# Kernel optimization log

Measured on AMD Instinct MI355X. Metric: run time of the kernel, lower is better.

Reference implementation:

```python
import jax, jax.numpy as jnp
import numpy as np

B, N, M, H, D, DIM = 4, 2048, 512, 12, 64, 768
INNER = H * D
SCALE = D ** -0.5
NEG = -1e9
TEMP = 24.0


def setup_inputs() -> dict:
    key = jax.random.key(0)
    ks = jax.random.split(key, 8)
    x = jax.random.normal(ks[0], (B, N, DIM), jnp.float32)
    kx = jax.random.normal(ks[1], (B, M, DIM), jnp.float32)
    krd = jax.random.uniform(ks[2], (B, H, M, N), jnp.float32)
    clst = jax.random.normal(ks[3], (B, 1, DIM), jnp.float32)
    att_mask = jax.random.randint(ks[4], (B, H, N, M), 0, 2) > 0
    W_qkv = jax.random.normal(ks[5], (DIM, 3 * INNER), jnp.float32) / np.sqrt(DIM)
    W_out = jax.random.normal(ks[6], (INNER, DIM), jnp.float32) / np.sqrt(INNER)
    b_out = jnp.zeros((DIM,), jnp.float32)
    return {"x": x, "kx": kx, "krd": krd, "clst": clst, "att_mask": att_mask,
            "W_qkv": W_qkv, "W_out": W_out, "b_out": b_out}


def _qkv(t, W_qkv):
    # [b, n, dim] -> three [b, h, n, d]
    b, n, _ = t.shape
    qkv = (t @ W_qkv).reshape(b, n, 3, H, D)
    qkv = jnp.moveaxis(qkv, 2, 0)            # [3, b, n, h, d]
    qkv = jnp.transpose(qkv, (0, 1, 3, 2, 4))  # [3, b, h, n, d]
    return qkv[0], qkv[1], qkv[2]


def _merge(t):
    # [b, h, n, d] -> [b, n, h*d]
    b, h, n, d = t.shape
    return jnp.transpose(t, (0, 2, 1, 3)).reshape(b, n, h * d)


def reference(x, kx, krd, clst, att_mask, W_qkv, W_out, b_out):
    t_q, t_k, t_v = _qkv(x, W_qkv)
    k_q, k_k, k_v = _qkv(kx, W_qkv)
    c_q, _, _ = _qkv(clst, W_qkv)

    krd_T = jnp.transpose(krd, (0, 1, 3, 2))  # [b, h, N, M]

    # branch 1: instance queries vs kernel keys
    dots = jnp.einsum('bhid,bhjd->bhij', t_q, k_k) * SCALE
    dots = jnp.where(att_mask, NEG, dots)
    attn_hot = jax.nn.softmax(dots * TEMP, axis=-1) * krd_T
    attn = jax.nn.softmax(dots, axis=-1) * krd_T
    att_out = _merge(jnp.einsum('bhij,bhjd->bhid', attn, k_v))

    # branch 2: kernel queries vs instance keys
    k_dots = jnp.einsum('bhid,bhjd->bhij', k_q, t_k) * SCALE
    k_dots = jnp.where(jnp.transpose(att_mask, (0, 1, 3, 2)), NEG, k_dots)
    k_attn = jax.nn.softmax(k_dots, axis=-1) * krd
    k_out = _merge(jnp.einsum('bhij,bhjd->bhid', k_attn, t_v))

    # branch 3: cluster query vs kernel keys
    c_dots = jnp.einsum('bhid,bhjd->bhij', c_q, k_k) * SCALE
    c_dots = jnp.where(att_mask[:, :, :1], NEG, c_dots)
    c_attn = jax.nn.softmax(c_dots, axis=-1)
    c_out = _merge(jnp.einsum('bhij,bhjd->bhid', c_attn, k_v))

    proj = lambda t: t @ W_out + b_out
    return (proj(att_out), proj(k_out), proj(c_out),
            jnp.transpose(attn_hot, (0, 1, 3, 2)))
```

## Files before the change

kernel.cpp:

```cpp
#include <hip/hip_runtime.h>
#include <hip/hip_bf16.h>
#include <cmath>
#include <cstdint>

#define B_ 4
#define N_ 2048
#define M_ 512
#define H_ 12
#define D_ 64
#define DIM_ 768
#define QKV_ 2304
#define SCALE_ 0.125f
#define NEG_ -1e9f
#define TEMP_ 24.0f
#define NSPLIT_ 4

typedef __attribute__((ext_vector_type(8))) short bf16x8;
typedef __attribute__((ext_vector_type(4))) float f32x4;

__device__ __forceinline__ short f2bf(float f) {
  union { float f; unsigned u; } v; v.f = f;
  unsigned r = v.u + 0x7fffu + ((v.u >> 16) & 1u);
  return (short)(r >> 16);
}
__device__ __forceinline__ float bf2f(short s) {
  union { unsigned u; float f; } v; v.u = ((unsigned)(unsigned short)s) << 16;
  return v.f;
}
#define MFMA16(a, b, c) __builtin_amdgcn_mfma_f32_16x16x32_bf16(a, b, c, 0, 0, 0)

__device__ __forceinline__ int xcd_swizzle(int orig, int nwg) {
  int qd = nwg >> 3, r = nwg & 7;
  int xcd = orig & 7, pos = orig >> 3;
  return (xcd < r ? xcd * (qd + 1) : r * (qd + 1) + (xcd - r) * qd) + pos;
}

__global__ __launch_bounds__(256) void wsplit_t(
    const float* __restrict__ W, int K, int Ncols,
    short* __restrict__ Wt_h, short* __restrict__ Wt_l) {
  __shared__ float t[32][33];
  const int n0 = blockIdx.x * 32, k0 = blockIdx.y * 32;
  const int tid = threadIdx.x;
  for (int e = tid; e < 1024; e += 256) {
    int r = e >> 5, c = e & 31;
    t[r][c] = W[(size_t)(k0 + r) * Ncols + n0 + c];
  }
  __syncthreads();
  for (int e = tid; e < 1024; e += 256) {
    int r = e >> 5, c = e & 31;
    float f = t[c][r];
    short hi = f2bf(f);
    short lo = f2bf(f - bf2f(hi));
    size_t o = (size_t)(n0 + r) * K + k0 + c;
    Wt_h[o] = hi; Wt_l[o] = lo;
  }
}

__global__ __launch_bounds__(256) void fsplit(
    const float* __restrict__ in, short* __restrict__ ho,
    short* __restrict__ lo_, int n4) {
  int stride = gridDim.x * 256;
  for (int i = blockIdx.x * 256 + threadIdx.x; i < n4; i += stride) {
    float4 f = ((const float4*)in)[i];
    short h0 = f2bf(f.x), h1 = f2bf(f.y), h2 = f2bf(f.z), h3 = f2bf(f.w);
    short l0 = f2bf(f.x - bf2f(h0)), l1 = f2bf(f.y - bf2f(h1));
    short l2 = f2bf(f.z - bf2f(h2)), l3 = f2bf(f.w - bf2f(h3));
    ((short4*)ho)[i] = make_short4(h0, h1, h2, h3);
    ((short4*)lo_)[i] = make_short4(l0, l1, l2, l3);
  }
}

__global__ __launch_bounds__(256) void mask_pack(
    const int* __restrict__ mask, unsigned* __restrict__ pm) {
  const size_t total = (size_t)B_ * H_ * N_ * M_;
  const size_t stride = (size_t)gridDim.x * blockDim.x;
  const int lane = threadIdx.x & 63;
  for (size_t i = (size_t)blockIdx.x * blockDim.x + threadIdx.x; i < total;
       i += stride) {
    unsigned long long bal = __ballot(mask[i] != 0);
    if (lane == 0) *(unsigned long long*)(pm + (i >> 5)) = bal;
  }
}

__global__ __launch_bounds__(256) void qkv_mfma(
    const short* __restrict__ Ahp, const short* __restrict__ Alp,
    const short* __restrict__ Wth, const short* __restrict__ Wtl,
    int rowsPerB, int totalRows,
    short* __restrict__ qh, short* __restrict__ ql,
    short* __restrict__ kh, short* __restrict__ kl,
    short* __restrict__ vt) {
  __shared__ __align__(16) short As_h[128 * 40], As_l[128 * 40];
  __shared__ __align__(16) short Bs_h[128 * 40], Bs_l[128 * 40];
  const int nwg = gridDim.x * gridDim.y;
  const int nb = xcd_swizzle(blockIdx.y * gridDim.x + blockIdx.x, nwg);
  const int gx = gridDim.x;
  const int r0 = (nb / gx) * 128, c0 = (nb % gx) * 128;
  const int tid = threadIdx.x;
  const int w = tid >> 6, ln = tid & 63, q = ln >> 4, l15 = ln & 15;
  const int wM = (w & 1) * 64, wN = (w >> 1) * 64;
  const f32x4 z = {0.f, 0.f, 0.f, 0.f};
  f32x4 acc[4][4];
  for (int i = 0; i < 4; i++)
    for (int j = 0; j < 4; j++) acc[i][j] = z;
  for (int k0 = 0; k0 < DIM_; k0 += 32) {
    for (int e = tid; e < 512; e += 256) {
      int row = e >> 2, c = e & 3;
      int ar = r0 + row; if (ar >= totalRows) ar = totalRows - 1;
      size_t ga = (size_t)ar * DIM_ + k0 + c * 8;
      size_t gb = (size_t)(c0 + row) * DIM_ + k0 + c * 8;
      int o = row * 40 + c * 8;
      *(uint4*)(As_h + o) = *(const uint4*)(Ahp + ga);
      *(uint4*)(As_l + o) = *(const uint4*)(Alp + ga);
      *(uint4*)(Bs_h + o) = *(const uint4*)(Wth + gb);
      *(uint4*)(Bs_l + o) = *(const uint4*)(Wtl + gb);
    }
    __syncthreads();
    bf16x8 ah[4], al[4], bhf[4], blf[4];
    for (int mt = 0; mt < 4; mt++) {
      int o = (wM + mt * 16 + l15) * 40 + q * 8;
      ah[mt] = *(const bf16x8*)(As_h + o);
      al[mt] = *(const bf16x8*)(As_l + o);
    }
    for (int nt = 0; nt < 4; nt++) {
      int o = (wN + nt * 16 + l15) * 40 + q * 8;
      bhf[nt] = *(const bf16x8*)(Bs_h + o);
      blf[nt] = *(const bf16x8*)(Bs_l + o);
    }
    for (int mt = 0; mt < 4; mt++)
      for (int nt = 0; nt < 4; nt++) {
        f32x4 c = acc[mt][nt];
        c = MFMA16(ah[mt], bhf[nt], c);
        c = MFMA16(ah[mt], blf[nt], c);
        c = MFMA16(al[mt], bhf[nt], c);
        acc[mt][nt] = c;
      }
    __syncthreads();
  }
  for (int mt = 0; mt < 4; mt++)
    for (int nt = 0; nt < 4; nt++)
      for (int r = 0; r < 4; r++) {
        int gr = r0 + wM + mt * 16 + q * 4 + r;
        if (gr >= totalRows) continue;
        int gc = c0 + wN + nt * 16 + l15;
        int which = gc / DIM_;
        int rem = gc - which * DIM_;
        int hh = rem >> 6, d = rem & 63;
        int b = gr / rowsPerB, n = gr - b * rowsPerB;
        float v = acc[mt][nt][r];
        short hi = f2bf(v);
        if (which == 2) {
          vt[(((size_t)b * H_ + hh) * 64 + d) * rowsPerB + n] = hi;
        } else {
          short lo = f2bf(v - bf2f(hi));
          size_t o = (((size_t)b * H_ + hh) * rowsPerB + n) * 64 + d;
          if (which == 0) { qh[o] = hi; ql[o] = lo; }
          else           { kh[o] = hi; kl[o] = lo; }
        }
      }
}

__global__ __launch_bounds__(256) void proj_mfma(
    const short* __restrict__ Ahp, const short* __restrict__ Alp,
    const short* __restrict__ Bth, const short* __restrict__ Btl,
    const float* __restrict__ bias, float* __restrict__ C, int totalRows) {
  __shared__ __align__(16) short As_h[128 * 40], As_l[128 * 40];
  __shared__ __align__(16) short Bs_h[128 * 40], Bs_l[128 * 40];
  const int nwg = gridDim.x * gridDim.y;
  const int nb = xcd_swizzle(blockIdx.y * gridDim.x + blockIdx.x, nwg);
  const int gx = gridDim.x;
  const int r0 = (nb / gx) * 128, c0 = (nb % gx) * 128;
  const int tid = threadIdx.x;
  const int w = tid >> 6, ln = tid & 63, q = ln >> 4, l15 = ln & 15;
  const int wM = (w & 1) * 64, wN = (w >> 1) * 64;
  const f32x4 z = {0.f, 0.f, 0.f, 0.f};
  f32x4 acc[4][4];
  for (int i = 0; i < 4; i++)
    for (int j = 0; j < 4; j++) acc[i][j] = z;
  for (int k0 = 0; k0 < DIM_; k0 += 32) {
    for (int e = tid; e < 512; e += 256) {
      int row = e >> 2, c = e & 3;
      int ar = r0 + row; if (ar >= totalRows) ar = totalRows - 1;
      size_t ga = (size_t)ar * DIM_ + k0 + c * 8;
      size_t gb = (size_t)(c0 + row) * DIM_ + k0 + c * 8;
      int o = row * 40 + c * 8;
      *(uint4*)(As_h + o) = *(const uint4*)(Ahp + ga);
      *(uint4*)(As_l + o) = *(const uint4*)(Alp + ga);
      *(uint4*)(Bs_h + o) = *(const uint4*)(Bth + gb);
      *(uint4*)(Bs_l + o) = *(const uint4*)(Btl + gb);
    }
    __syncthreads();
    bf16x8 ah[4], al[4], bhf[4], blf[4];
    for (int mt = 0; mt < 4; mt++) {
      int o = (wM + mt * 16 + l15) * 40 + q * 8;
      ah[mt] = *(const bf16x8*)(As_h + o);
      al[mt] = *(const bf16x8*)(As_l + o);
    }
    for (int nt = 0; nt < 4; nt++) {
      int o = (wN + nt * 16 + l15) * 40 + q * 8;
      bhf[nt] = *(const bf16x8*)(Bs_h + o);
      blf[nt] = *(const bf16x8*)(Bs_l + o);
    }
    for (int mt = 0; mt < 4; mt++)
      for (int nt = 0; nt < 4; nt++) {
        f32x4 c = acc[mt][nt];
        c = MFMA16(ah[mt], bhf[nt], c);
        c = MFMA16(ah[mt], blf[nt], c);
        c = MFMA16(al[mt], bhf[nt], c);
        acc[mt][nt] = c;
      }
    __syncthreads();
  }
  for (int mt = 0; mt < 4; mt++)
    for (int nt = 0; nt < 4; nt++)
      for (int r = 0; r < 4; r++) {
        int gr = r0 + wM + mt * 16 + q * 4 + r;
        if (gr >= totalRows) continue;
        int gc = c0 + wN + nt * 16 + l15;
        C[(size_t)gr * DIM_ + gc] = acc[mt][nt][r] + bias[gc];
      }
}

__global__ __launch_bounds__(512, 4) void branch1_mfma(
    const short* __restrict__ tqh, const short* __restrict__ tql,
    const short* __restrict__ kkh, const short* __restrict__ kkl,
    const short* __restrict__ kvt, const float* __restrict__ krd,
    const unsigned* __restrict__ pm, float* __restrict__ out3,
    short* __restrict__ amh, short* __restrict__ aml) {
  __shared__ __align__(16) float sc[32 * 520];
  __shared__ unsigned mskw[512];
  __shared__ float rowM[32], inv1[32], inv2[32];
  short* P2h = (short*)sc;
  short* P2l = P2h + 32 * 520;
  const int b = blockIdx.z, h = blockIdx.y, n0 = blockIdx.x * 32;
  const size_t bhi = (size_t)b * H_ + h;
  const int tid = threadIdx.x;
  const int w = tid >> 6, ln = tid & 63, q = ln >> 4, l15 = ln & 15;
  const float* krd0 = krd + bhi * M_ * N_;
  mskw[tid] = pm[(bhi * N_ + n0) * 16 + tid];
  {
    bf16x8 ah[2][2], al[2][2];
    for (int mt = 0; mt < 2; mt++) {
      const short* ap = tqh + ((bhi * N_ + n0 + mt * 16 + l15) * D_ + q * 8);
      const short* ap2 = tql + ((bhi * N_ + n0 + mt * 16 + l15) * D_ + q * 8);
      ah[mt][0] = *(const bf16x8*)(ap);
      ah[mt][1] = *(const bf16x8*)(ap + 32);
      al[mt][0] = *(const bf16x8*)(ap2);
      al[mt][1] = *(const bf16x8*)(ap2 + 32);
    }
    for (int t = 0; t < 4; t++) {
      int ct = w * 4 + t;
      const short* bp = kkh + ((bhi * M_ + ct * 16 + l15) * D_ + q * 8);
      const short* bp2 = kkl + ((bhi * M_ + ct * 16 + l15) * D_ + q * 8);
      bf16x8 bh0 = *(const bf16x8*)(bp);
      bf16x8 bh1 = *(const bf16x8*)(bp + 32);
      bf16x8 bl0 = *(const bf16x8*)(bp2);
      bf16x8 bl1 = *(const bf16x8*)(bp2 + 32);
      for (int mt = 0; mt < 2; mt++) {
        f32x4 a = {0.f, 0.f, 0.f, 0.f};
        a = MFMA16(ah[mt][0], bh0, a); a = MFMA16(ah[mt][1], bh1, a);
        a = MFMA16(ah[mt][0], bl0, a); a = MFMA16(ah[mt][1], bl1, a);
        a = MFMA16(al[mt][0], bh0, a); a = MFMA16(al[mt][1], bh1, a);
        for (int r = 0; r < 4; r++) {
          int row = mt * 16 + q * 4 + r;
          sc[row * 520 + ((ct * 16 + l15) ^ ((row >> 2) & 7))] = a[r];
        }
      }
    }
  }
  const int pi = tid & 31, pg = tid >> 5;
  float kr[32];
#pragma unroll
  for (int t = 0; t < 32; t++)
    kr[t] = __builtin_nontemporal_load(
        krd0 + (size_t)(pg * 32 + t) * N_ + n0 + pi);
  __syncthreads();
  {
    int i = tid >> 4, jl = tid & 15;
    int sw = (i >> 2) & 7;
    float* scr = sc + i * 520;
    const unsigned* mrow = mskw + i * 16;
    float mx = -INFINITY;
    for (int j = jl; j < M_; j += 16) {
      float dv = scr[j ^ sw];
      dv = ((mrow[j >> 5] >> (j & 31)) & 1) ? NEG_ : dv * SCALE_;
      scr[j ^ sw] = dv;
      mx = fmaxf(mx, dv);
    }
    for (int o = 8; o >= 1; o >>= 1) mx = fmaxf(mx, __shfl_xor(mx, o, 16));
    float s1 = 0.f, s2 = 0.f;
    for (int j = jl; j < M_; j += 16) {
      float e2 = __expf(scr[j ^ sw] - mx);
      scr[j ^ sw] = e2;
      float x2 = e2 * e2, x4 = x2 * x2, x8 = x4 * x4, x16 = x8 * x8;
      s1 += x16 * x8;
      s2 += e2;
    }
    for (int o = 8; o >= 1; o >>= 1) {
      s1 += __shfl_xor(s1, o, 16);
      s2 += __shfl_xor(s2, o, 16);
    }
    if (jl == 0) { inv1[i] = 1.f / s1; inv2[i] = 1.f / s2; }
  }
  __syncthreads();
  {
    float rv[32];
    int sw2 = (pi >> 2) & 7;
#pragma unroll
    for (int t = 0; t < 32; t++)
      rv[t] = sc[pi * 520 + ((pg * 32 + t) ^ sw2)];
    __syncthreads();
    float v1 = inv1[pi], v2 = inv2[pi];
    float* o3 = out3 + bhi * M_ * N_ + n0 + pi;
#pragma unroll
    for (int t = 0; t < 32; t += 2) {
      int j = pg * 32 + t;
      float e2a = rv[t], e2b = rv[t + 1];
      float a2 = e2a * e2a, a4 = a2 * a2, a8 = a4 * a4, a16 = a8 * a8;
      float b2 = e2b * e2b, b4 = b2 * b2, b8 = b4 * b4, b16 = b8 * b8;
      __builtin_nontemporal_store(a16 * a8 * v1 * kr[t], o3 + (size_t)j * N_);
      __builtin_nontemporal_store(b16 * b8 * v1 * kr[t + 1],
                                  o3 + (size_t)(j + 1) * N_);
      float p0 = e2a * v2 * kr[t];
      float p1 = e2b * v2 * kr[t + 1];
      short h0 = f2bf(p0), h1 = f2bf(p1);
      short lo0 = f2bf(p0 - bf2f(h0)), lo1 = f2bf(p1 - bf2f(h1));
      *(short2*)(P2h + pi * 520 + j) = make_short2(h0, h1);
      *(short2*)(P2l + pi * 520 + j) = make_short2(lo0, lo1);
    }
  }
  __syncthreads();
  {
    const int dc = w & 3, nh = w >> 2;
    f32x4 o0 = {0.f, 0.f, 0.f, 0.f}, o1 = {0.f, 0.f, 0.f, 0.f};
    const short* vbase = kvt + ((bhi * 64 + dc * 16 + l15) * (size_t)M_ + q * 8);
    const short* ph = P2h + (nh * 16 + l15) * 520 + q * 8;
    const short* pl = P2l + (nh * 16 + l15) * 520 + q * 8;
    for (int kc = 0; kc < 16; kc += 2) {
      bf16x8 pa0 = *(const bf16x8*)(ph + kc * 32);
      bf16x8 pl0 = *(const bf16x8*)(pl + kc * 32);
      bf16x8 bv0 = *(const bf16x8*)(vbase + kc * 32);
      o0 = MFMA16(pa0, bv0, o0);
      o0 = MFMA16(pl0, bv0, o0);
      bf16x8 pa1 = *(const bf16x8*)(ph + (kc + 1) * 32);
      bf16x8 pl1 = *(const bf16x8*)(pl + (kc + 1) * 32);
      bf16x8 bv1 = *(const bf16x8*)(vbase + (kc + 1) * 32);
      o1 = MFMA16(pa1, bv1, o1);
      o1 = MFMA16(pl1, bv1, o1);
    }
    o0 += o1;
    for (int r = 0; r < 4; r++) {
      float v = o0[r];
      short hi = f2bf(v), lo = f2bf(v - bf2f(hi));
      size_t o = ((size_t)b * N_ + n0 + nh * 16 + q * 4 + r) * DIM_ +
                 h * 64 + dc * 16 + l15;
      amh[o] = hi; aml[o] = lo;
    }
  }
}

__global__ __launch_bounds__(256) void branch2_mfma(
    const short* __restrict__ kqh, const short* __restrict__ kql,
    const short* __restrict__ tkh, const short* __restrict__ tkl,
    const short* __restrict__ tvt, const float* __restrict__ krd,
    const unsigned* __restrict__ pm, float* __restrict__ pO,
    float* __restrict__ pML) {
  __shared__ __align__(16) float sc[32 * 136];
  __shared__ unsigned mskw[128];
  __shared__ float rowM[32], rowL[32], alph[32];
  short* P2h = (short*)sc;
  short* P2l = P2h + 32 * 136;
  const int b = blockIdx.z, h = blockIdx.y;
  const int mblk = blockIdx.x >> 2, split = blockIdx.x & 3;
  const int m0 = mblk * 32;
  const size_t bhi = (size_t)b * H_ + h;
  const int pidx = ((int)bhi * 16 + mblk) * NSPLIT_ + split;
  const int tid = threadIdx.x;
  const int w = tid >> 6, ln = tid & 63, q = ln >> 4, l15 = ln & 15;
  const float* krd0 = krd + (bhi * M_ + m0) * N_;
  const int mword = m0 >> 5;
  bf16x8 Ah[2][2], Al[2][2];
  for (int mt = 0; mt < 2; mt++)
    for (int kc = 0; kc < 2; kc++) {
      size_t o = (bhi * M_ + m0 + mt * 16 + l15) * D_ + kc * 32 + q * 8;
      Ah[mt][kc] = *(const bf16x8*)(kqh + o);
      Al[mt][kc] = *(const bf16x8*)(kql + o);
    }
  if (tid < 32) { rowM[tid] = -INFINITY; rowL[tid] = 0.f; }
  const f32x4 z = {0.f, 0.f, 0.f, 0.f};
  f32x4 oa[2]; oa[0] = z; oa[1] = z;
  __syncthreads();
  const int nbeg = split * (N_ / NSPLIT_), nend = nbeg + N_ / NSPLIT_;
  for (int n0 = nbeg; n0 < nend; n0 += 128) {
    if (tid < 128) mskw[tid] = pm[(bhi * N_ + n0 + tid) * 16 + mword];
    for (int t = 0; t < 2; t++) {
      int ct = w * 2 + t;
      const short* bp = tkh + ((bhi * N_ + n0 + ct * 16 + l15) * D_ + q * 8);
      const short* bp2 = tkl + ((bhi * N_ + n0 + ct * 16 + l15) * D_ + q * 8);
      bf16x8 bh0 = *(const bf16x8*)(bp), bh1 = *(const bf16x8*)(bp + 32);
      bf16x8 bl0 = *(const bf16x8*)(bp2), bl1 = *(const bf16x8*)(bp2 + 32);
      for (int mt = 0; mt < 2; mt++) {
        f32x4 a = {0.f, 0.f, 0.f, 0.f};
        a = MFMA16(Ah[mt][0], bh0, a); a = MFMA16(Ah[mt][1], bh1, a);
        a = MFMA16(Ah[mt][0], bl0, a); a = MFMA16(Ah[mt][1], bl1, a);
        a = MFMA16(Al[mt][0], bh0, a); a = MFMA16(Al[mt][1], bh1, a);
        for (int r = 0; r < 4; r++)
          sc[(mt * 16 + q * 4 + r) * 136 + ct * 16 + l15] = a[r];
      }
    }
    __syncthreads();
    {
      int i = tid >> 3, jl = tid & 7;
      float mx = -INFINITY;
      for (int j = jl; j < 128; j += 8) {
        float s = sc[i * 136 + j];
        s = ((mskw[j] >> i) & 1) ? NEG_ : s * SCALE_;
        sc[i * 136 + j] = s;
        mx = fmaxf(mx, s);
      }
      for (int o = 4; o >= 1; o >>= 1) mx = fmaxf(mx, __shfl_xor(mx, o, 8));
      float mold = rowM[i];
      float mnew = fmaxf(mold, mx);
      float sum = 0.f;
      for (int j = jl; j < 128; j += 8) {
        float p = __expf(sc[i * 136 + j] - mnew);
        sc[i * 136 + j] = p;
        sum += p;
      }
      for (int o = 4; o >= 1; o >>= 1) sum += __shfl_xor(sum, o, 8);
      if (jl == 0) {
        float al = (mold == -INFINITY) ? 0.f : __expf(mold - mnew);
        alph[i] = al;
        rowL[i] = rowL[i] * al + sum;
        rowM[i] = mnew;
      }
    }
    __syncthreads();
    {
      float rv[16], kv2[16];
      const int j = tid & 127;
      const int ib = tid >> 7;
#pragma unroll
      for (int t = 0; t < 16; t++) {
        rv[t] = sc[(ib + 2 * t) * 136 + j];
        kv2[t] = __builtin_nontemporal_load(
            krd0 + (size_t)(ib + 2 * t) * N_ + n0 + j);
      }
      __syncthreads();
#pragma unroll
      for (int t = 0; t < 16; t++) {
        int i = ib + 2 * t;
        float p2 = rv[t] * kv2[t];
        short hi = f2bf(p2), lo = f2bf(p2 - bf2f(hi));
        P2h[i * 136 + j] = hi;
        P2l[i * 136 + j] = lo;
      }
    }
    __syncthreads();
    {
      for (int mt = 0; mt < 2; mt++) {
        f32x4 t = oa[mt];
        for (int r = 0; r < 4; r++) t[r] *= alph[mt * 16 + q * 4 + r];
        for (int kc = 0; kc < 4; kc++) {
          bf16x8 pa = *(const bf16x8*)(P2h + (mt * 16 + l15) * 136 + kc * 32 + q * 8);
          bf16x8 pl = *(const bf16x8*)(P2l + (mt * 16 + l15) * 136 + kc * 32 + q * 8);
          bf16x8 bv = *(const bf16x8*)(tvt + ((bhi * 64 + w * 16 + l15) * (size_t)N_ + n0 + kc * 32 + q * 8));
          t = MFMA16(pa, bv, t);
          t = MFMA16(pl, bv, t);
        }
        oa[mt] = t;
      }
    }
    __syncthreads();
  }
  float* po = pO + (size_t)pidx * 2048;
  for (int mt = 0; mt < 2; mt++)
    for (int r = 0; r < 4; r++) {
      int row = mt * 16 + q * 4 + r;
      po[row * 64 + w * 16 + l15] = oa[mt][r];
    }
  if (tid < 32) {
    pML[(size_t)pidx * 64 + tid] = rowM[tid];
    pML[(size_t)pidx * 64 + 32 + tid] = rowL[tid];
  }
}

__global__ __launch_bounds__(256) void b2_combine(
    const float* __restrict__ pO, const float* __restrict__ pML,
    short* __restrict__ kmh, short* __restrict__ kml) {
  const int mblk = blockIdx.x, h = blockIdx.y, b = blockIdx.z;
  const size_t bhi = (size_t)b * H_ + h;
  const int base = ((int)bhi * 16 + mblk) * NSPLIT_;
  __shared__ float mS[NSPLIT_][32], lS[NSPLIT_][32], wgt[NSPLIT_][32], invL[32];
  const int tid = threadIdx.x;
  if (tid < 32 * NSPLIT_) {
    int s = tid >> 5, r = tid & 31;
    mS[s][r] = pML[(size_t)(base + s) * 64 + r];
    lS[s][r] = pML[(size_t)(base + s) * 64 + 32 + r];
  }
  __syncthreads();
  if (tid < 32) {
    float Mv = mS[0][tid];
    for (int s = 1; s < NSPLIT_; s++) Mv = fmaxf(Mv, mS[s][tid]);
    float L = 0.f;
    for (int s = 0; s < NSPLIT_; s++) {
      float wv = __expf(mS[s][tid] - Mv);
      wgt[s][tid] = wv;
      L += lS[s][tid] * wv;
    }
    invL[tid] = 1.f / L;
  }
  __syncthreads();
  const int row = tid >> 3, c0 = (tid & 7) * 8;
  float acc[8] = {0, 0, 0, 0, 0, 0, 0, 0};
  for (int s = 0; s < NSPLIT_; s++) {
    float wv = wgt[s][row];
    const float* src = pO + (size_t)(base + s) * 2048 + row * 64 + c0;
    float4 a = *(const float4*)(src);
    float4 bq = *(const float4*)(src + 4);
    acc[0] += a.x * wv;  acc[1] += a.y * wv;
    acc[2] += a.z * wv;  acc[3] += a.w * wv;
    acc[4] += bq.x * wv; acc[5] += bq.y * wv;
    acc[6] += bq.z * wv; acc[7] += bq.w * wv;
  }
  float il = invL[row];
  size_t o = ((size_t)b * M_ + mblk * 32 + row) * DIM_ + h * 64 + c0;
#pragma unroll
  for (int e = 0; e < 8; e++) {
    float v = acc[e] * il;
    short hi = f2bf(v), lo = f2bf(v - bf2f(hi));
    kmh[o + e] = hi; kml[o + e] = lo;
  }
}

__global__ __launch_bounds__(256) void branch3_k(
    const short* __restrict__ cqh, const short* __restrict__ cql,
    const short* __restrict__ kkh, const short* __restrict__ kkl,
    const short* __restrict__ kvt, const unsigned* __restrict__ pm,
    short* __restrict__ cmh, short* __restrict__ cml) {
  const int h = blockIdx.x, b = blockIdx.y;
  __shared__ float qv[64];
  __shared__ float p[512];
  __shared__ float wr1[4], wr2[4];
  __shared__ float ored[4][64];
  const size_t bhi = (size_t)b * H_ + h;
  const int tid = threadIdx.x;
  if (tid < 64) qv[tid] = bf2f(cqh[bhi * 64 + tid]) + bf2f(cql[bhi * 64 + tid]);
  __syncthreads();
  const unsigned* m0p = pm + bhi * N_ * 16;
  for (int j = tid; j < 512; j += 256) {
    float acc = 0;
    for (int kk = 0; kk < 64; kk++)
      acc += qv[kk] * (bf2f(kkh[(bhi * M_ + j) * 64 + kk]) +
                       bf2f(kkl[(bhi * M_ + j) * 64 + kk]));
    acc *= SCALE_;
    if ((m0p[j >> 5] >> (j & 31)) & 1) acc = NEG_;
    p[j] = acc;
  }
  __syncthreads();
  float mx = fmaxf(p[tid], p[tid + 256]);
  for (int o = 32; o >= 1; o >>= 1) mx = fmaxf(mx, __shfl_xor(mx, o, 64));
  if ((tid & 63) == 0) wr1[tid >> 6] = mx;
  __syncthreads();
  mx = fmaxf(fmaxf(wr1[0], wr1[1]), fmaxf(wr1[2], wr1[3]));
  float e0 = __expf(p[tid] - mx), e1 = __expf(p[tid + 256] - mx);
  float s = e0 + e1;
  for (int o = 32; o >= 1; o >>= 1) s += __shfl_xor(s, o, 64);
  p[tid] = e0; p[tid + 256] = e1;
  if ((tid & 63) == 0) wr2[tid >> 6] = s;
  __syncthreads();
  float invS = 1.f / (wr2[0] + wr2[1] + wr2[2] + wr2[3]);
  int dd = tid & 63, gg = tid >> 6;
  float o = 0;
  for (int j = gg; j < 512; j += 4)
    o += p[j] * bf2f(kvt[(bhi * 64 + dd) * (size_t)M_ + j]);
  ored[gg][dd] = o;
  __syncthreads();
  if (gg == 0) {
    float r = (ored[0][dd] + ored[1][dd] + ored[2][dd] + ored[3][dd]) * invS;
    short hi = f2bf(r), lo = f2bf(r - bf2f(hi));
    cmh[(size_t)b * DIM_ + h * 64 + dd] = hi;
    cml[(size_t)b * DIM_ + h * 64 + dd] = lo;
  }
}

extern "C" void kernel_launch(void* const* d_in, const int* in_sizes, int n_in,
                              void* d_out, int out_size, void* d_ws,
                              size_t ws_size, hipStream_t stream) {
  const float* x = (const float*)d_in[0];
  const float* kx = (const float*)d_in[1];
  const float* krd = (const float*)d_in[2];
  const float* clst = (const float*)d_in[3];
  const int* mask = (const int*)d_in[4];
  const float* Wqkv = (const float*)d_in[5];
  const float* Wout = (const float*)d_in[6];
  const float* bout = (const float*)d_in[7];

  short* p = (short*)d_ws;
  auto alloc = [&](size_t n) { short* r = p; p += n; return r; };
  short* Wq_h = alloc(2304ull * 768); short* Wq_l = alloc(2304ull * 768);
  short* Wo_h = alloc(768ull * 768);  short* Wo_l = alloc(768ull * 768);
  short* tq_h = alloc(6291456); short* tq_l = alloc(6291456);
  short* tk_h = alloc(6291456); short* tk_l = alloc(6291456);
  short* tv_t = alloc(6291456);
  short* kq_h = alloc(1572864); short* kq_l = alloc(1572864);
  short* kk_h = alloc(1572864); short* kk_l = alloc(1572864);
  short* kv_t = alloc(1572864);
  short* cq_h = alloc(3072); short* cq_l = alloc(3072);
  short* ck_h = alloc(3072); short* ck_l = alloc(3072);
  short* cv_t = alloc(3072);
  short* am_h = alloc(6291456); short* am_l = alloc(6291456);
  short* km_h = alloc(1572864); short* km_l = alloc(1572864);
  short* cm_h = alloc(3072); short* cm_l = alloc(3072);

  float* out0 = (float*)d_out;
  float* out1 = out0 + 6291456;
  float* out2 = out1 + 1572864;
  float* out3 = out2 + 3072;

  wsplit_t<<<dim3(72, 24), 256, 0, stream>>>(Wqkv, DIM_, QKV_, Wq_h, Wq_l);
  wsplit_t<<<dim3(24, 24), 256, 0, stream>>>(Wout, DIM_, DIM_, Wo_h, Wo_l);

  short* xs_h = am_h, *xs_l = am_l;
  short* kxs_h = km_h, *kxs_l = km_l;
  short* cs_h = cm_h, *cs_l = cm_l;
  fsplit<<<dim3(2048), 256, 0, stream>>>(x, xs_h, xs_l, B_ * N_ * DIM_ / 4);
  fsplit<<<dim3(1536), 256, 0, stream>>>(kx, kxs_h, kxs_l, B_ * M_ * DIM_ / 4);
  fsplit<<<dim3(3), 256, 0, stream>>>(clst, cs_h, cs_l, B_ * DIM_ / 4);

  qkv_mfma<<<dim3(18, 64), 256, 0, stream>>>(xs_h, xs_l, Wq_h, Wq_l, N_,
                                             B_ * N_, tq_h, tq_l, tk_h, tk_l,
                                             tv_t);
  qkv_mfma<<<dim3(18, 16), 256, 0, stream>>>(kxs_h, kxs_l, Wq_h, Wq_l, M_,
                                             B_ * M_, kq_h, kq_l, kk_h, kk_l,
                                             kv_t);
  qkv_mfma<<<dim3(18, 1), 256, 0, stream>>>(cs_h, cs_l, Wq_h, Wq_l, 1, B_,
                                            cq_h, cq_l, ck_h, ck_l, cv_t);

  unsigned* pmask = (unsigned*)Wq_h;
  mask_pack<<<dim3(2048), 256, 0, stream>>>(mask, pmask);

  branch1_mfma<<<dim3(N_ / 32, H_, B_), 512, 0, stream>>>(
      tq_h, tq_l, kk_h, kk_l, kv_t, krd, pmask, out3, am_h, am_l);

  float* pO = out0;
  float* pML = out1;
  branch2_mfma<<<dim3((M_ / 32) * NSPLIT_, H_, B_), 256, 0, stream>>>(
      kq_h, kq_l, tk_h, tk_l, tv_t, krd, pmask, pO, pML);
  b2_combine<<<dim3(M_ / 32, H_, B_), 256, 0, stream>>>(pO, pML, km_h, km_l);

  branch3_k<<<dim3(H_, B_), 256, 0, stream>>>(cq_h, cq_l, kk_h, kk_l, kv_t,
                                              pmask, cm_h, cm_l);

  proj_mfma<<<dim3(6, 64), 256, 0, stream>>>(am_h, am_l, Wo_h, Wo_l, bout,
                                             out0, B_ * N_);
  proj_mfma<<<dim3(6, 16), 256, 0, stream>>>(km_h, km_l, Wo_h, Wo_l, bout,
                                             out1, B_ * M_);
  proj_mfma<<<dim3(6, 1), 256, 0, stream>>>(cm_h, cm_l, Wo_h, Wo_l, bout,
                                            out2, B_);
}
```

Before: 1.168 ms.

## Merge launches, use direct global-to-LDS loads, double branch-2 splits

```diff
diff --git a/kernel.cpp b/kernel.cpp
--- a/kernel.cpp
+++ b/kernel.cpp
@@ -13,7 +13,7 @@
 #define SCALE_ 0.125f
 #define NEG_ -1e9f
 #define TEMP_ 24.0f
-#define NSPLIT_ 4
+#define NSPLIT_ 8
 
 typedef __attribute__((ext_vector_type(8))) short bf16x8;
 typedef __attribute__((ext_vector_type(4))) float f32x4;
@@ -29,17 +29,29 @@
 }
 #define MFMA16(a, b, c) __builtin_amdgcn_mfma_f32_16x16x32_bf16(a, b, c, 0, 0, 0)
 
+__device__ __forceinline__ void gl16(const void* g, void* l) {
+  __builtin_amdgcn_global_load_lds(
+      (const __attribute__((address_space(1))) unsigned int*)g,
+      (__attribute__((address_space(3))) unsigned int*)l, 16, 0, 0);
+}
+
 __device__ __forceinline__ int xcd_swizzle(int orig, int nwg) {
   int qd = nwg >> 3, r = nwg & 7;
   int xcd = orig & 7, pos = orig >> 3;
   return (xcd < r ? xcd * (qd + 1) : r * (qd + 1) + (xcd - r) * qd) + pos;
 }
 
-__global__ __launch_bounds__(256) void wsplit_t(
-    const float* __restrict__ W, int K, int Ncols,
-    short* __restrict__ Wt_h, short* __restrict__ Wt_l) {
+__global__ __launch_bounds__(256) void wsplit_all(
+    const float* __restrict__ Wqkv, const float* __restrict__ Wout,
+    short* __restrict__ Wqh, short* __restrict__ Wql,
+    short* __restrict__ Woh, short* __restrict__ Wol) {
   __shared__ float t[32][33];
-  const int n0 = blockIdx.x * 32, k0 = blockIdx.y * 32;
+  int bx = blockIdx.x;
+  const float* W; int Ncols; short *Wh, *Wl;
+  if (bx < 72) { W = Wqkv; Ncols = QKV_; Wh = Wqh; Wl = Wql; }
+  else { bx -= 72; W = Wout; Ncols = DIM_; Wh = Woh; Wl = Wol; }
+  const int K = DIM_;
+  const int n0 = bx * 32, k0 = blockIdx.y * 32;
   const int tid = threadIdx.x;
   for (int e = tid; e < 1024; e += 256) {
     int r = e >> 5, c = e & 31;
@@ -52,21 +64,32 @@
     short hi = f2bf(f);
     short lo = f2bf(f - bf2f(hi));
     size_t o = (size_t)(n0 + r) * K + k0 + c;
-    Wt_h[o] = hi; Wt_l[o] = lo;
-  }
-}
-
-__global__ __launch_bounds__(256) void fsplit(
-    const float* __restrict__ in, short* __restrict__ ho,
-    short* __restrict__ lo_, int n4) {
+    Wh[o] = hi; Wl[o] = lo;
+  }
+}
+
+__global__ __launch_bounds__(256) void fsplit_all(
+    const float* __restrict__ x, const float* __restrict__ kx,
+    const float* __restrict__ c,
+    short* __restrict__ xh, short* __restrict__ xl,
+    short* __restrict__ kh2, short* __restrict__ kl2,
+    short* __restrict__ ch, short* __restrict__ cl) {
+  const int XN4 = B_ * N_ * DIM_ / 4;
+  const int KN4 = B_ * M_ * DIM_ / 4;
+  const int CN4 = B_ * DIM_ / 4;
+  const int total = XN4 + KN4 + CN4;
   int stride = gridDim.x * 256;
-  for (int i = blockIdx.x * 256 + threadIdx.x; i < n4; i += stride) {
-    float4 f = ((const float4*)in)[i];
+  for (int i = blockIdx.x * 256 + threadIdx.x; i < total; i += stride) {
+    const float* src; short *ho, *lo2; int idx;
+    if (i < XN4) { src = x; ho = xh; lo2 = xl; idx = i; }
+    else if (i < XN4 + KN4) { src = kx; ho = kh2; lo2 = kl2; idx = i - XN4; }
+    else { src = c; ho = ch; lo2 = cl; idx = i - XN4 - KN4; }
+    float4 f = ((const float4*)src)[idx];
     short h0 = f2bf(f.x), h1 = f2bf(f.y), h2 = f2bf(f.z), h3 = f2bf(f.w);
     short l0 = f2bf(f.x - bf2f(h0)), l1 = f2bf(f.y - bf2f(h1));
     short l2 = f2bf(f.z - bf2f(h2)), l3 = f2bf(f.w - bf2f(h3));
-    ((short4*)ho)[i] = make_short4(h0, h1, h2, h3);
-    ((short4*)lo_)[i] = make_short4(l0, l1, l2, l3);
+    ((short4*)ho)[idx] = make_short4(h0, h1, h2, h3);
+    ((short4*)lo2)[idx] = make_short4(l0, l1, l2, l3);
   }
 }
 
@@ -82,19 +105,36 @@
   }
 }
 
-__global__ __launch_bounds__(256) void qkv_mfma(
-    const short* __restrict__ Ahp, const short* __restrict__ Alp,
+__global__ __launch_bounds__(256) void qkv_all(
+    const short* __restrict__ xsh, const short* __restrict__ xsl,
+    const short* __restrict__ kxsh, const short* __restrict__ kxsl,
+    const short* __restrict__ csh, const short* __restrict__ csl,
     const short* __restrict__ Wth, const short* __restrict__ Wtl,
-    int rowsPerB, int totalRows,
-    short* __restrict__ qh, short* __restrict__ ql,
-    short* __restrict__ kh, short* __restrict__ kl,
-    short* __restrict__ vt) {
-  __shared__ __align__(16) short As_h[128 * 40], As_l[128 * 40];
-  __shared__ __align__(16) short Bs_h[128 * 40], Bs_l[128 * 40];
-  const int nwg = gridDim.x * gridDim.y;
-  const int nb = xcd_swizzle(blockIdx.y * gridDim.x + blockIdx.x, nwg);
-  const int gx = gridDim.x;
-  const int r0 = (nb / gx) * 128, c0 = (nb % gx) * 128;
+    short* __restrict__ tqh, short* __restrict__ tql,
+    short* __restrict__ tkh, short* __restrict__ tkl, short* __restrict__ tvt,
+    short* __restrict__ kqh, short* __restrict__ kql,
+    short* __restrict__ kkh, short* __restrict__ kkl, short* __restrict__ kvt,
+    short* __restrict__ cqh, short* __restrict__ cql,
+    short* __restrict__ ckh, short* __restrict__ ckl, short* __restrict__ cvt) {
+  __shared__ __align__(16) short As_h[128 * 32], As_l[128 * 32];
+  __shared__ __align__(16) short Bs_h[128 * 32], Bs_l[128 * 32];
+  int flat = blockIdx.y * 18 + blockIdx.x;
+  flat = xcd_swizzle(flat, 18 * 81);
+  int by = flat / 18, bx = flat % 18;
+  const short *Ahp, *Alp; int rowsPerB, totalRows, r0;
+  short *qh, *ql, *kh, *kl, *vt;
+  if (by < 64) {
+    Ahp = xsh; Alp = xsl; rowsPerB = N_; totalRows = B_ * N_; r0 = by * 128;
+    qh = tqh; ql = tql; kh = tkh; kl = tkl; vt = tvt;
+  } else if (by < 80) {
+    Ahp = kxsh; Alp = kxsl; rowsPerB = M_; totalRows = B_ * M_;
+    r0 = (by - 64) * 128;
+    qh = kqh; ql = kql; kh = kkh; kl = kkl; vt = kvt;
+  } else {
+    Ahp = csh; Alp = csl; rowsPerB = 1; totalRows = B_; r0 = 0;
+    qh = cqh; ql = cql; kh = ckh; kl = ckl; vt = cvt;
+  }
+  const int c0 = bx * 128;
   const int tid = threadIdx.x;
   const int w = tid >> 6, ln = tid & 63, q = ln >> 4, l15 = ln & 15;
   const int wM = (w & 1) * 64, wN = (w >> 1) * 64;
@@ -108,31 +148,30 @@
       int ar = r0 + row; if (ar >= totalRows) ar = totalRows - 1;
       size_t ga = (size_t)ar * DIM_ + k0 + c * 8;
       size_t gb = (size_t)(c0 + row) * DIM_ + k0 + c * 8;
-      int o = row * 40 + c * 8;
-      *(uint4*)(As_h + o) = *(const uint4*)(Ahp + ga);
-      *(uint4*)(As_l + o) = *(const uint4*)(Alp + ga);
-      *(uint4*)(Bs_h + o) = *(const uint4*)(Wth + gb);
-      *(uint4*)(Bs_l + o) = *(const uint4*)(Wtl + gb);
+      gl16(Ahp + ga, As_h + e * 8);
+      gl16(Alp + ga, As_l + e * 8);
+      gl16(Wth + gb, Bs_h + e * 8);
+      gl16(Wtl + gb, Bs_l + e * 8);
     }
     __syncthreads();
     bf16x8 ah[4], al[4], bhf[4], blf[4];
     for (int mt = 0; mt < 4; mt++) {
-      int o = (wM + mt * 16 + l15) * 40 + q * 8;
+      int o = (wM + mt * 16 + l15) * 32 + q * 8;
       ah[mt] = *(const bf16x8*)(As_h + o);
       al[mt] = *(const bf16x8*)(As_l + o);
     }
     for (int nt = 0; nt < 4; nt++) {
-      int o = (wN + nt * 16 + l15) * 40 + q * 8;
+      int o = (wN + nt * 16 + l15) * 32 + q * 8;
       bhf[nt] = *(const bf16x8*)(Bs_h + o);
       blf[nt] = *(const bf16x8*)(Bs_l + o);
     }
     for (int mt = 0; mt < 4; mt++)
       for (int nt = 0; nt < 4; nt++) {
-        f32x4 c = acc[mt][nt];
-        c = MFMA16(ah[mt], bhf[nt], c);
-        c = MFMA16(ah[mt], blf[nt], c);
-        c = MFMA16(al[mt], bhf[nt], c);
-        acc[mt][nt] = c;
+        f32x4 cc = acc[mt][nt];
+        cc = MFMA16(ah[mt], bhf[nt], cc);
+        cc = MFMA16(ah[mt], blf[nt], cc);
+        cc = MFMA16(al[mt], bhf[nt], cc);
+        acc[mt][nt] = cc;
       }
     __syncthreads();
   }
@@ -159,16 +198,23 @@
       }
 }
 
-__global__ __launch_bounds__(256) void proj_mfma(
-    const short* __restrict__ Ahp, const short* __restrict__ Alp,
+__global__ __launch_bounds__(256) void proj_all(
+    const short* __restrict__ amh, const short* __restrict__ aml,
+    const short* __restrict__ kmh, const short* __restrict__ kml,
+    const short* __restrict__ cmh, const short* __restrict__ cml,
     const short* __restrict__ Bth, const short* __restrict__ Btl,
-    const float* __restrict__ bias, float* __restrict__ C, int totalRows) {
-  __shared__ __align__(16) short As_h[128 * 40], As_l[128 * 40];
-  __shared__ __align__(16) short Bs_h[128 * 40], Bs_l[128 * 40];
-  const int nwg = gridDim.x * gridDim.y;
-  const int nb = xcd_swizzle(blockIdx.y * gridDim.x + blockIdx.x, nwg);
-  const int gx = gridDim.x;
-  const int r0 = (nb / gx) * 128, c0 = (nb % gx) * 128;
+    const float* __restrict__ bias, float* __restrict__ out0,
+    float* __restrict__ out1, float* __restrict__ out2) {
+  __shared__ __align__(16) short As_h[128 * 32], As_l[128 * 32];
+  __shared__ __align__(16) short Bs_h[128 * 32], Bs_l[128 * 32];
+  int flat = blockIdx.y * 6 + blockIdx.x;
+  flat = xcd_swizzle(flat, 6 * 81);
+  int by = flat / 6, bx = flat % 6;
+  const short *Ahp, *Alp; int totalRows, r0; float* C;
+  if (by < 64) { Ahp = amh; Alp = aml; totalRows = B_ * N_; r0 = by * 128; C = out0; }
+  else if (by < 80) { Ahp = kmh; Alp = kml; totalRows = B_ * M_; r0 = (by - 64) * 128; C = out1; }
+  else { Ahp = cmh; Alp = cml; totalRows = B_; r0 = 0; C = out2; }
+  const int c0 = bx * 128;
   const int tid = threadIdx.x;
   const int w = tid >> 6, ln = tid & 63, q = ln >> 4, l15 = ln & 15;
   const int wM = (w & 1) * 64, wN = (w >> 1) * 64;
@@ -182,31 +228,30 @@
       int ar = r0 + row; if (ar >= totalRows) ar = totalRows - 1;
       size_t ga = (size_t)ar * DIM_ + k0 + c * 8;
       size_t gb = (size_t)(c0 + row) * DIM_ + k0 + c * 8;
-      int o = row * 40 + c * 8;
-      *(uint4*)(As_h + o) = *(const uint4*)(Ahp + ga);
-      *(uint4*)(As_l + o) = *(const uint4*)(Alp + ga);
-      *(uint4*)(Bs_h + o) = *(const uint4*)(Bth + gb);
-      *(uint4*)(Bs_l + o) = *(const uint4*)(Btl + gb);
+      gl16(Ahp + ga, As_h + e * 8);
+      gl16(Alp + ga, As_l + e * 8);
+      gl16(Bth + gb, Bs_h + e * 8);
+      gl16(Btl + gb, Bs_l + e * 8);
     }
     __syncthreads();
     bf16x8 ah[4], al[4], bhf[4], blf[4];
     for (int mt = 0; mt < 4; mt++) {
-      int o = (wM + mt * 16 + l15) * 40 + q * 8;
+      int o = (wM + mt * 16 + l15) * 32 + q * 8;
       ah[mt] = *(const bf16x8*)(As_h + o);
       al[mt] = *(const bf16x8*)(As_l + o);
     }
     for (int nt = 0; nt < 4; nt++) {
-      int o = (wN + nt * 16 + l15) * 40 + q * 8;
+      int o = (wN + nt * 16 + l15) * 32 + q * 8;
       bhf[nt] = *(const bf16x8*)(Bs_h + o);
       blf[nt] = *(const bf16x8*)(Bs_l + o);
     }
     for (int mt = 0; mt < 4; mt++)
       for (int nt = 0; nt < 4; nt++) {
-        f32x4 c = acc[mt][nt];
-        c = MFMA16(ah[mt], bhf[nt], c);
-        c = MFMA16(ah[mt], blf[nt], c);
-        c = MFMA16(al[mt], bhf[nt], c);
-        acc[mt][nt] = c;
+        f32x4 cc = acc[mt][nt];
+        cc = MFMA16(ah[mt], bhf[nt], cc);
+        cc = MFMA16(ah[mt], blf[nt], cc);
+        cc = MFMA16(al[mt], bhf[nt], cc);
+        acc[mt][nt] = cc;
       }
     __syncthreads();
   }
@@ -228,7 +273,7 @@
     short* __restrict__ amh, short* __restrict__ aml) {
   __shared__ __align__(16) float sc[32 * 520];
   __shared__ unsigned mskw[512];
-  __shared__ float rowM[32], inv1[32], inv2[32];
+  __shared__ float inv1[32], inv2[32];
   short* P2h = (short*)sc;
   short* P2l = P2h + 32 * 520;
   const int b = blockIdx.z, h = blockIdx.y, n0 = blockIdx.x * 32;
@@ -279,17 +324,22 @@
     int sw = (i >> 2) & 7;
     float* scr = sc + i * 520;
     const unsigned* mrow = mskw + i * 16;
+    float dv[32];
     float mx = -INFINITY;
-    for (int j = jl; j < M_; j += 16) {
-      float dv = scr[j ^ sw];
-      dv = ((mrow[j >> 5] >> (j & 31)) & 1) ? NEG_ : dv * SCALE_;
-      scr[j ^ sw] = dv;
-      mx = fmaxf(mx, dv);
+#pragma unroll
+    for (int t = 0; t < 32; t++) {
+      int j = jl + 16 * t;
+      float d = scr[j ^ sw];
+      d = ((mrow[j >> 5] >> (j & 31)) & 1) ? NEG_ : d * SCALE_;
+      dv[t] = d;
+      mx = fmaxf(mx, d);
     }
     for (int o = 8; o >= 1; o >>= 1) mx = fmaxf(mx, __shfl_xor(mx, o, 16));
     float s1 = 0.f, s2 = 0.f;
-    for (int j = jl; j < M_; j += 16) {
-      float e2 = __expf(scr[j ^ sw] - mx);
+#pragma unroll
+    for (int t = 0; t < 32; t++) {
+      int j = jl + 16 * t;
+      float e2 = __expf(dv[t] - mx);
       scr[j ^ sw] = e2;
       float x2 = e2 * e2, x4 = x2 * x2, x8 = x4 * x4, x16 = x8 * x8;
       s1 += x16 * x8;
@@ -365,19 +415,20 @@
     const unsigned* __restrict__ pm, float* __restrict__ pO,
     float* __restrict__ pML) {
   __shared__ __align__(16) float sc[32 * 136];
+  __shared__ __align__(16) float krdL[32 * 128];
   __shared__ unsigned mskw[128];
   __shared__ float rowM[32], rowL[32], alph[32];
   short* P2h = (short*)sc;
   short* P2l = P2h + 32 * 136;
   const int b = blockIdx.z, h = blockIdx.y;
-  const int mblk = blockIdx.x >> 2, split = blockIdx.x & 3;
+  const int mblk = blockIdx.x >> 3, split = blockIdx.x & 7;
   const int m0 = mblk * 32;
   const size_t bhi = (size_t)b * H_ + h;
   const int pidx = ((int)bhi * 16 + mblk) * NSPLIT_ + split;
   const int tid = threadIdx.x;
   const int w = tid >> 6, ln = tid & 63, q = ln >> 4, l15 = ln & 15;
   const float* krd0 = krd + (bhi * M_ + m0) * N_;
-  const int mword = m0 >> 5;
+  const int mword = mblk;
   bf16x8 Ah[2][2], Al[2][2];
   for (int mt = 0; mt < 2; mt++)
     for (int kc = 0; kc < 2; kc++) {
@@ -389,9 +440,13 @@
   const f32x4 z = {0.f, 0.f, 0.f, 0.f};
   f32x4 oa[2]; oa[0] = z; oa[1] = z;
   __syncthreads();
-  const int nbeg = split * (N_ / NSPLIT_), nend = nbeg + N_ / NSPLIT_;
-  for (int n0 = nbeg; n0 < nend; n0 += 128) {
+  const int nbeg = split * (N_ / NSPLIT_);
+  for (int n0 = nbeg; n0 < nbeg + N_ / NSPLIT_; n0 += 128) {
     if (tid < 128) mskw[tid] = pm[(bhi * N_ + n0 + tid) * 16 + mword];
+    for (int e = tid; e < 1024; e += 256) {
+      int row = e >> 5, c = e & 31;
+      gl16(krd0 + (size_t)row * N_ + n0 + c * 4, krdL + e * 4);
+    }
     for (int t = 0; t < 2; t++) {
       int ct = w * 2 + t;
       const short* bp = tkh + ((bhi * N_ + n0 + ct * 16 + l15) * D_ + q * 8);
@@ -436,20 +491,16 @@
     }
     __syncthreads();
     {
-      float rv[16], kv2[16];
+      float rv[16];
       const int j = tid & 127;
       const int ib = tid >> 7;
 #pragma unroll
-      for (int t = 0; t < 16; t++) {
-        rv[t] = sc[(ib + 2 * t) * 136 + j];
-        kv2[t] = __builtin_nontemporal_load(
-            krd0 + (size_t)(ib + 2 * t) * N_ + n0 + j);
-      }
+      for (int t = 0; t < 16; t++) rv[t] = sc[(ib + 2 * t) * 136 + j];
       __syncthreads();
 #pragma unroll
       for (int t = 0; t < 16; t++) {
         int i = ib + 2 * t;
-        float p2 = rv[t] * kv2[t];
+        float p2 = rv[t] * krdL[i * 128 + j];
         short hi = f2bf(p2), lo = f2bf(p2 - bf2f(hi));
         P2h[i * 136 + j] = hi;
         P2l[i * 136 + j] = lo;
@@ -492,7 +543,7 @@
   const int base = ((int)bhi * 16 + mblk) * NSPLIT_;
   __shared__ float mS[NSPLIT_][32], lS[NSPLIT_][32], wgt[NSPLIT_][32], invL[32];
   const int tid = threadIdx.x;
-  if (tid < 32 * NSPLIT_) {
+  {
     int s = tid >> 5, r = tid & 31;
     mS[s][r] = pML[(size_t)(base + s) * 64 + r];
     lS[s][r] = pML[(size_t)(base + s) * 64 + 32 + r];
@@ -617,44 +668,36 @@
   float* out2 = out1 + 1572864;
   float* out3 = out2 + 3072;
 
-  wsplit_t<<<dim3(72, 24), 256, 0, stream>>>(Wqkv, DIM_, QKV_, Wq_h, Wq_l);
-  wsplit_t<<<dim3(24, 24), 256, 0, stream>>>(Wout, DIM_, DIM_, Wo_h, Wo_l);
+  wsplit_all<<<dim3(96, 24), 256, 0, stream>>>(Wqkv, Wout, Wq_h, Wq_l,
+                                               Wo_h, Wo_l);
 
   short* xs_h = am_h, *xs_l = am_l;
   short* kxs_h = km_h, *kxs_l = km_l;
   short* cs_h = cm_h, *cs_l = cm_l;
-  fsplit<<<dim3(2048), 256, 0, stream>>>(x, xs_h, xs_l, B_ * N_ * DIM_ / 4);
-  fsplit<<<dim3(1536), 256, 0, stream>>>(kx, kxs_h, kxs_l, B_ * M_ * DIM_ / 4);
-  fsplit<<<dim3(3), 256, 0, stream>>>(clst, cs_h, cs_l, B_ * DIM_ / 4);
-
-  qkv_mfma<<<dim3(18, 64), 256, 0, stream>>>(xs_h, xs_l, Wq_h, Wq_l, N_,
-                                             B_ * N_, tq_h, tq_l, tk_h, tk_l,
-                                             tv_t);
-  qkv_mfma<<<dim3(18, 16), 256, 0, stream>>>(kxs_h, kxs_l, Wq_h, Wq_l, M_,
-                                             B_ * M_, kq_h, kq_l, kk_h, kk_l,
-                                             kv_t);
-  qkv_mfma<<<dim3(18, 1), 256, 0, stream>>>(cs_h, cs_l, Wq_h, Wq_l, 1, B_,
-                                            cq_h, cq_l, ck_h, ck_l, cv_t);
+  fsplit_all<<<dim3(2048), 256, 0, stream>>>(x, kx, clst, xs_h, xs_l,
+                                             kxs_h, kxs_l, cs_h, cs_l);
+
+  qkv_all<<<dim3(18, 81), 256, 0, stream>>>(
+      xs_h, xs_l, kxs_h, kxs_l, cs_h, cs_l, Wq_h, Wq_l,
+      tq_h, tq_l, tk_h, tk_l, tv_t,
+      kq_h, kq_l, kk_h, kk_l, kv_t,
+      cq_h, cq_l, ck_h, ck_l, cv_t);
 
   unsigned* pmask = (unsigned*)Wq_h;
   mask_pack<<<dim3(2048), 256, 0, stream>>>(mask, pmask);
 
-  branch1_mfma<<<dim3(N_ / 32, H_, B_), 512, 0, stream>>>(
-      tq_h, tq_l, kk_h, kk_l, kv_t, krd, pmask, out3, am_h, am_l);
-
-  float* pO = out0;
-  float* pML = out1;
+  float* pO = out3;
+  float* pML = out3 + 12582912;
   branch2_mfma<<<dim3((M_ / 32) * NSPLIT_, H_, B_), 256, 0, stream>>>(
       kq_h, kq_l, tk_h, tk_l, tv_t, krd, pmask, pO, pML);
   b2_combine<<<dim3(M_ / 32, H_, B_), 256, 0, stream>>>(pO, pML, km_h, km_l);
 
+  branch1_mfma<<<dim3(N_ / 32, H_, B_), 512, 0, stream>>>(
+      tq_h, tq_l, kk_h, kk_l, kv_t, krd, pmask, out3, am_h, am_l);
+
   branch3_k<<<dim3(H_, B_), 256, 0, stream>>>(cq_h, cq_l, kk_h, kk_l, kv_t,
                                               pmask, cm_h, cm_l);
 
-  proj_mfma<<<dim3(6, 64), 256, 0, stream>>>(am_h, am_l, Wo_h, Wo_l, bout,
-                                             out0, B_ * N_);
-  proj_mfma<<<dim3(6, 16), 256, 0, stream>>>(km_h, km_l, Wo_h, Wo_l, bout,
-                                             out1, B_ * M_);
-  proj_mfma<<<dim3(6, 1), 256, 0, stream>>>(cm_h, cm_l, Wo_h, Wo_l, bout,
-                                            out2, B_);
-}
+  proj_all<<<dim3(6, 81), 256, 0, stream>>>(am_h, am_l, km_h, km_l, cm_h, cm_l,
+                                            Wo_h, Wo_l, bout, out0, out1, out2);
+}
```

Result: faster. 975.3 us (-16.5%).
